# Kernel optimization log

Hardware: AMD Instinct MI355X
Metric: run time of the kernel (lower is better)

The kernel has to match this reference:

```python
import jax, jax.numpy as jnp
import numpy as np


def _conv1x1(x, w, b):
    # x: [B, Cin, H, W]; w: [Cout, Cin, 1, 1]; b: [Cout]
    y = jnp.einsum('bchw,oc->bohw', x, w[:, :, 0, 0])
    return y + b[None, :, None, None]


def setup_inputs() -> dict:
    key = jax.random.key(0)
    ks = jax.random.split(key, 9)
    B, C, H, W = 8, 256, 64, 64
    Cq = C // 4
    sc = 0.05
    return {
        'x': jax.random.normal(ks[0], (B, C, H, W), jnp.float32),
        'query_weight': jax.random.normal(ks[1], (Cq, C, 1, 1), jnp.float32) * sc,
        'query_bias': jax.random.normal(ks[2], (Cq,), jnp.float32) * sc,
        'key_weight': jax.random.normal(ks[3], (Cq, C, 1, 1), jnp.float32) * sc,
        'key_bias': jax.random.normal(ks[4], (Cq,), jnp.float32) * sc,
        'value_weight': jax.random.normal(ks[5], (C, C, 1, 1), jnp.float32) * sc,
        'value_bias': jax.random.normal(ks[6], (C,), jnp.float32) * sc,
        'gamma_weight': jax.random.normal(ks[7], (C, C, 1, 1), jnp.float32) * sc,
        'gamma_bias': jax.random.normal(ks[8], (C,), jnp.float32) * sc,
    }


def reference(x, query_weight, query_bias, key_weight, key_bias,
              value_weight, value_bias, gamma_weight, gamma_bias):
    B, C, H, W = x.shape
    N = H * W
    q = _conv1x1(x, query_weight, query_bias).reshape(B, -1, N)   # [B, Cq, N]
    k = _conv1x1(x, key_weight, key_bias).reshape(B, -1, N)       # [B, Cq, N]
    v = _conv1x1(x, value_weight, value_bias).reshape(B, C, N)    # [B, C, N]
    # energy[b, i, j] = sum_c q[b, c, i] * k[b, c, j]
    energy = jnp.einsum('bci,bcj->bij', q, k)                     # [B, N, N]
    energy = jax.nn.elu(energy) / N
    out = jnp.einsum('bcn,bnm->bcm', v, energy).reshape(B, C, H, W)
    return _conv1x1(out, gamma_weight, gamma_bias)
```

## Files before the change

kernel.cpp:

```cpp
#include <hip/hip_runtime.h>
#include <cmath>

#define BB 8
#define CC 256
#define CQ 64
#define NN 4096
#define VROW 4224
constexpr float INV_N = 1.0f / 4096.0f;

typedef __attribute__((ext_vector_type(8))) short short8;
typedef __attribute__((ext_vector_type(4))) short short4v;
typedef __attribute__((ext_vector_type(4))) float float4v;

__device__ __forceinline__ short f2bf(float f) {
  union { float f; unsigned u; } x; x.f = f;
  unsigned r = x.u + 0x7fffu + ((x.u >> 16) & 1u);
  return (short)(r >> 16);
}

__device__ __forceinline__ void lds_barrier() {
  asm volatile("s_waitcnt lgkmcnt(0)" ::: "memory");
  __builtin_amdgcn_s_barrier();
  __builtin_amdgcn_sched_barrier(0);
}

__global__ void wconv_kernel(const float* __restrict__ wq,
                             const float* __restrict__ wk,
                             short* __restrict__ wqb, short* __restrict__ wkb) {
  const int t = blockIdx.x * 256 + threadIdx.x;
  const float* src; short* dst; int idx;
  if (t < 4096) { src = wq; dst = wqb; idx = t; }
  else          { src = wk; dst = wkb; idx = t - 4096; }
  const float4 v = *reinterpret_cast<const float4*>(&src[(size_t)idx * 4]);
  short4v o;
  o[0] = f2bf(v.x); o[1] = f2bf(v.y); o[2] = f2bf(v.z); o[3] = f2bf(v.w);
  *reinterpret_cast<short4v*>(&dst[(size_t)idx * 4]) = o;
}

__global__ void wprep_kernel(const float* __restrict__ wg,
                             const float* __restrict__ wv,
                             const float* __restrict__ bv,
                             short* __restrict__ wvpb, float* __restrict__ bvp) {
  const int o = blockIdx.x, t = threadIdx.x;
  float s = 0.f;
  for (int c = 0; c < 256; ++c)
    s += wg[(size_t)o * 256 + c] * wv[(size_t)c * 256 + t];
  wvpb[(size_t)o * 256 + t] = f2bf(s);

  __shared__ float red[256];
  red[t] = wg[(size_t)o * 256 + t] * bv[t];
  __syncthreads();
  for (int off = 128; off; off >>= 1) {
    if (t < off) red[t] += red[t + off];
    __syncthreads();
  }
  if (t == 0) bvp[o] = red[0];
}

__global__ __launch_bounds__(256, 2) void qkv_kernel(
    const float* __restrict__ X,
    const short* __restrict__ wqb, const float* __restrict__ bq,
    const short* __restrict__ wkb, const float* __restrict__ bk,
    const short* __restrict__ wvpb, const float* __restrict__ bvp,
    short* __restrict__ qt, short* __restrict__ kt, short* __restrict__ vbf) {
  __shared__ short xt[64 * 264];
  const int tid = threadIdx.x;
  const int wid = tid >> 6;
  const int lane = tid & 63, quad = lane >> 4, l16 = lane & 15;
  const int b = blockIdx.x, n0 = blockIdx.y * 64;

  float4 xb[16];
#pragma unroll
  for (int p = 0; p < 16; ++p) {
    const int idx = p * 256 + tid;
    const int c = idx >> 4;
    const int n4 = (idx & 15) * 4;
    xb[p] = *reinterpret_cast<const float4*>(
        &X[((size_t)b * CC + c) * NN + n0 + n4]);
  }
#pragma unroll
  for (int p = 0; p < 16; ++p) {
    const int idx = p * 256 + tid;
    const int c = idx >> 4;
    const int n4 = (idx & 15) * 4;
    xt[(n4 + 0) * 264 + c] = f2bf(xb[p].x);
    xt[(n4 + 1) * 264 + c] = f2bf(xb[p].y);
    xt[(n4 + 2) * 264 + c] = f2bf(xb[p].z);
    xt[(n4 + 3) * 264 + c] = f2bf(xb[p].w);
  }
  __syncthreads();

  short8 bfr[8][4];
#pragma unroll
  for (int kk = 0; kk < 8; ++kk)
#pragma unroll
    for (int tm = 0; tm < 4; ++tm)
      bfr[kk][tm] = *reinterpret_cast<const short8*>(
          &xt[(tm * 16 + l16) * 264 + kk * 32 + quad * 8]);
  __syncthreads();

  short* Os0 = xt;
  short* Os1 = xt + 4608;

  for (int ch = 0; ch < 6; ++ch) {
    const short* W; const float* bias; int obase;
    if (ch == 0)      { W = wqb; bias = bq; obase = 0; }
    else if (ch == 1) { W = wkb; bias = bk; obase = 0; }
    else { W = wvpb + (size_t)(ch - 2) * 64 * CC; bias = bvp + (ch - 2) * 64; obase = (ch - 2) * 64; }

    const short* wrow = &W[(size_t)(wid * 16 + l16) * CC + quad * 8];
    short8 wf[8];
#pragma unroll
    for (int kk = 0; kk < 8; ++kk)
      wf[kk] = *reinterpret_cast<const short8*>(wrow + kk * 32);

    float4v acc[4];
#pragma unroll
    for (int tm = 0; tm < 4; ++tm) acc[tm] = float4v{0.f, 0.f, 0.f, 0.f};
#pragma unroll
    for (int kk = 0; kk < 8; ++kk)
#pragma unroll
      for (int tm = 0; tm < 4; ++tm)
        acc[tm] = __builtin_amdgcn_mfma_f32_16x16x32_bf16(wf[kk], bfr[kk][tm], acc[tm], 0, 0, 0);

    if (ch < 2) {
      short* dst = (ch == 0) ? qt : kt;
#pragma unroll
      for (int tm = 0; tm < 4; ++tm) {
        short4v pk;
#pragma unroll
        for (int r = 0; r < 4; ++r)
          pk[r] = f2bf(acc[tm][r] + bias[wid * 16 + quad * 4 + r]);
        *reinterpret_cast<short4v*>(
            &dst[((size_t)b * NN + n0 + tm * 16 + l16) * 64 + wid * 16 + quad * 4]) = pk;
      }
    } else {
      short* Os = (ch & 1) ? Os1 : Os0;
#pragma unroll
      for (int tm = 0; tm < 4; ++tm)
#pragma unroll
        for (int r = 0; r < 4; ++r)
          Os[(wid * 16 + quad * 4 + r) * 72 + tm * 16 + l16] =
              f2bf(acc[tm][r] + bias[wid * 16 + quad * 4 + r]);
      __syncthreads();
      const int o = tid >> 2, ng = (tid & 3) * 16;
      const int orow = obase + o;
      const short8 s0 = *reinterpret_cast<const short8*>(&Os[o * 72 + ng]);
      const short8 s1 = *reinterpret_cast<const short8*>(&Os[o * 72 + ng + 8]);
      short* vp = &vbf[((size_t)b * CC + orow) * VROW + n0 + ng];
      *reinterpret_cast<short8*>(vp) = s0;
      *reinterpret_cast<short8*>(vp + 8) = s1;
    }
  }
}

__global__ __launch_bounds__(256, 2) void attn_kernel(
    const short* __restrict__ qt, const short* __restrict__ kt,
    const short* __restrict__ vbf, const float* __restrict__ bg,
    float* __restrict__ out) {
  __shared__ short smem[9216];
  short* Es0 = smem;
  short* Es1 = smem + 4608;

  const int tid = threadIdx.x;
  const int wid = tid >> 6;
  const int lane = tid & 63, quad = lane >> 4, l16 = lane & 15;
  const int b = blockIdx.x, m0 = blockIdx.y * 64;

  short8 bkf[4][2];
#pragma unroll
  for (int tm = 0; tm < 4; ++tm)
#pragma unroll
    for (int kk = 0; kk < 2; ++kk)
      bkf[tm][kk] = *reinterpret_cast<const short8*>(
          &kt[((size_t)b * NN + m0 + tm * 16 + l16) * 64 + kk * 32 + quad * 8]);

  const short* qp = &qt[((size_t)b * NN + wid * 16 + l16) * 64 + quad * 8];
  const short* vrow[4];
#pragma unroll
  for (int tc = 0; tc < 4; ++tc) {
    const int crow = wid * 64 + tc * 16 + l16;
    vrow[tc] = &vbf[((size_t)b * CC + crow) * VROW + quad * 8];
  }

  float4v acc[4][4];
#pragma unroll
  for (int i = 0; i < 4; ++i)
#pragma unroll
    for (int j = 0; j < 4; ++j) acc[i][j] = float4v{0.f, 0.f, 0.f, 0.f};

  short8 avA[4][2], avB[4][2];
#pragma unroll
  for (int tc = 0; tc < 4; ++tc) {
    avA[tc][0] = *reinterpret_cast<const short8*>(vrow[tc]);
    avA[tc][1] = *reinterpret_cast<const short8*>(vrow[tc] + 32);
  }
  short8 aqA0 = *reinterpret_cast<const short8*>(qp + (size_t)1 * 4096);
  short8 aqA1 = *reinterpret_cast<const short8*>(qp + (size_t)1 * 4096 + 32);
  short8 aqB0, aqB1;
  {
    const short8 aq0 = *reinterpret_cast<const short8*>(qp);
    const short8 aq1 = *reinterpret_cast<const short8*>(qp + 32);
#pragma unroll
    for (int tm = 0; tm < 4; ++tm) {
      float4v t = {0.f, 0.f, 0.f, 0.f};
      t = __builtin_amdgcn_mfma_f32_16x16x32_bf16(aq0, bkf[tm][0], t, 0, 0, 0);
      t = __builtin_amdgcn_mfma_f32_16x16x32_bf16(aq1, bkf[tm][1], t, 0, 0, 0);
      short4v pk;
#pragma unroll
      for (int r = 0; r < 4; ++r) {
        float sv = t[r];
        sv = (sv > 0.f) ? sv : (__expf(sv) - 1.f);
        pk[r] = f2bf(sv);
      }
      *reinterpret_cast<short4v*>(
          &Es0[(tm * 16 + l16) * 72 + wid * 16 + quad * 4]) = pk;
    }
  }
  lds_barrier();

  auto seg = [&](int it, short8 (&avc)[4][2], short8 (&avn)[4][2],
                 short8& aqc0, short8& aqc1, short8& aqn0, short8& aqn1) {
    const int nb1 = (it + 1) * 64;
#pragma unroll
    for (int tc = 0; tc < 4; ++tc) {
      avn[tc][0] = *reinterpret_cast<const short8*>(vrow[tc] + nb1);
      avn[tc][1] = *reinterpret_cast<const short8*>(vrow[tc] + nb1 + 32);
    }
    aqn0 = *reinterpret_cast<const short8*>(qp + (size_t)(it + 2) * 4096);
    aqn1 = *reinterpret_cast<const short8*>(qp + (size_t)(it + 2) * 4096 + 32);

    short* Esr = (it & 1) ? Es1 : Es0;
    short* Esw = (it & 1) ? Es0 : Es1;

    float4v s[4];
    if (it < 63) {
#pragma unroll
      for (int tm = 0; tm < 4; ++tm) {
        float4v t = {0.f, 0.f, 0.f, 0.f};
        t = __builtin_amdgcn_mfma_f32_16x16x32_bf16(aqc0, bkf[tm][0], t, 0, 0, 0);
        t = __builtin_amdgcn_mfma_f32_16x16x32_bf16(aqc1, bkf[tm][1], t, 0, 0, 0);
        s[tm] = t;
      }
    }

#pragma unroll
    for (int tm = 0; tm < 4; ++tm) {
      const short8 be0 = *reinterpret_cast<const short8*>(
          &Esr[(tm * 16 + l16) * 72 + quad * 8]);
      const short8 be1 = *reinterpret_cast<const short8*>(
          &Esr[(tm * 16 + l16) * 72 + 32 + quad * 8]);
#pragma unroll
      for (int tc = 0; tc < 4; ++tc) {
        acc[tc][tm] = __builtin_amdgcn_mfma_f32_16x16x32_bf16(avc[tc][0], be0, acc[tc][tm], 0, 0, 0);
        acc[tc][tm] = __builtin_amdgcn_mfma_f32_16x16x32_bf16(avc[tc][1], be1, acc[tc][tm], 0, 0, 0);
      }
    }

    if (it < 63) {
#pragma unroll
      for (int tm = 0; tm < 4; ++tm) {
        short4v pk;
#pragma unroll
        for (int r = 0; r < 4; ++r) {
          float sv = s[tm][r];
          sv = (sv > 0.f) ? sv : (__expf(sv) - 1.f);
          pk[r] = f2bf(sv);
        }
        *reinterpret_cast<short4v*>(
            &Esw[(tm * 16 + l16) * 72 + wid * 16 + quad * 4]) = pk;
      }
    }
    lds_barrier();
  };

  for (int it = 0; it < 64; it += 2) {
    seg(it,     avA, avB, aqA0, aqA1, aqB0, aqB1);
    seg(it + 1, avB, avA, aqB0, aqB1, aqA0, aqA1);
  }

#pragma unroll
  for (int tc = 0; tc < 4; ++tc) {
#pragma unroll
    for (int r = 0; r < 4; ++r) {
      const int o = wid * 64 + tc * 16 + quad * 4 + r;
      const float bgv = bg[o];
#pragma unroll
      for (int tm = 0; tm < 4; ++tm) {
        out[((size_t)b * CC + o) * NN + m0 + tm * 16 + l16] =
            acc[tc][tm][r] * INV_N + bgv;
      }
    }
  }
}

extern "C" void kernel_launch(void* const* d_in, const int* in_sizes, int n_in,
                              void* d_out, int out_size, void* d_ws,
                              size_t ws_size, hipStream_t stream) {
  const float* x  = (const float*)d_in[0];
  const float* wq = (const float*)d_in[1];
  const float* bq = (const float*)d_in[2];
  const float* wk = (const float*)d_in[3];
  const float* bk = (const float*)d_in[4];
  const float* wv = (const float*)d_in[5];
  const float* bv = (const float*)d_in[6];
  const float* wg = (const float*)d_in[7];
  const float* bg = (const float*)d_in[8];
  float* out = (float*)d_out;

  short* qt   = (short*)d_ws;
  short* kt   = qt + (size_t)BB * NN * CQ;
  short* vbf  = kt + (size_t)BB * NN * CQ;
  short* wqb  = vbf + (size_t)BB * CC * VROW;
  short* wkb  = wqb + (size_t)CQ * CC;
  short* wvpb = wkb + (size_t)CQ * CC;
  float* bvp  = (float*)(wvpb + (size_t)CC * CC);

  wconv_kernel<<<dim3(32), 256, 0, stream>>>(wq, wk, wqb, wkb);
  wprep_kernel<<<dim3(256), 256, 0, stream>>>(wg, wv, bv, wvpb, bvp);
  qkv_kernel<<<dim3(BB, NN / 64), 256, 0, stream>>>(x, wqb, bq, wkb, bk,
                                                    wvpb, bvp, qt, kt, vbf);
  attn_kernel<<<dim3(BB, NN / 64), 256, 0, stream>>>(qt, kt, vbf, bg, out);
}
```

Before: 274.7 us.

## Keep energy tiles in registers and drop LDS staging and barriers

The attention kernel no longer has its four waves cooperatively compute the energy tile, write it to double-buffered LDS and synchronise with barriers. Each wave now recomputes the whole 64x64 energy tile itself, loading Q rows in a permuted order so the MFMA output layout lines up with the B-operand layout of the next MFMA. This removes LDS traffic and block-wide barriers. In exchange each wave does four times the QK MFMA and exp work, and the software prefetch of V and Q into registers is gone.

After: 355.4 us. +29.4%, slower.

```diff
diff --git a/kernel.cpp b/kernel.cpp
--- a/kernel.cpp
+++ b/kernel.cpp
@@ -16,12 +16,6 @@
   union { float f; unsigned u; } x; x.f = f;
   unsigned r = x.u + 0x7fffu + ((x.u >> 16) & 1u);
   return (short)(r >> 16);
-}
-
-__device__ __forceinline__ void lds_barrier() {
-  asm volatile("s_waitcnt lgkmcnt(0)" ::: "memory");
-  __builtin_amdgcn_s_barrier();
-  __builtin_amdgcn_sched_barrier(0);
 }
 
 __global__ void wconv_kernel(const float* __restrict__ wq,
@@ -158,10 +152,6 @@
     const short* __restrict__ qt, const short* __restrict__ kt,
     const short* __restrict__ vbf, const float* __restrict__ bg,
     float* __restrict__ out) {
-  __shared__ short smem[9216];
-  short* Es0 = smem;
-  short* Es1 = smem + 4608;
-
   const int tid = threadIdx.x;
   const int wid = tid >> 6;
   const int lane = tid & 63, quad = lane >> 4, l16 = lane & 15;
@@ -171,17 +161,20 @@
 #pragma unroll
   for (int tm = 0; tm < 4; ++tm)
 #pragma unroll
-    for (int kk = 0; kk < 2; ++kk)
-      bkf[tm][kk] = *reinterpret_cast<const short8*>(
-          &kt[((size_t)b * NN + m0 + tm * 16 + l16) * 64 + kk * 32 + quad * 8]);
-
-  const short* qp = &qt[((size_t)b * NN + wid * 16 + l16) * 64 + quad * 8];
+    for (int ch = 0; ch < 2; ++ch)
+      bkf[tm][ch] = *reinterpret_cast<const short8*>(
+          &kt[((size_t)b * NN + m0 + tm * 16 + l16) * 64 + ch * 32 + quad * 8]);
+
+  int nperm[4];
+#pragma unroll
+  for (int ng = 0; ng < 4; ++ng)
+    nperm[ng] = (ng & 2) * 16 + (l16 >> 2) * 8 + (ng & 1) * 4 + (l16 & 3);
+  const short* qbase = &qt[(size_t)b * NN * 64 + quad * 8];
+
   const short* vrow[4];
 #pragma unroll
-  for (int tc = 0; tc < 4; ++tc) {
-    const int crow = wid * 64 + tc * 16 + l16;
-    vrow[tc] = &vbf[((size_t)b * CC + crow) * VROW + quad * 8];
-  }
+  for (int tc = 0; tc < 4; ++tc)
+    vrow[tc] = &vbf[((size_t)b * CC + wid * 64 + tc * 16 + l16) * VROW + quad * 8];
 
   float4v acc[4][4];
 #pragma unroll
@@ -189,94 +182,55 @@
 #pragma unroll
     for (int j = 0; j < 4; ++j) acc[i][j] = float4v{0.f, 0.f, 0.f, 0.f};
 
-  short8 avA[4][2], avB[4][2];
-#pragma unroll
-  for (int tc = 0; tc < 4; ++tc) {
-    avA[tc][0] = *reinterpret_cast<const short8*>(vrow[tc]);
-    avA[tc][1] = *reinterpret_cast<const short8*>(vrow[tc] + 32);
-  }
-  short8 aqA0 = *reinterpret_cast<const short8*>(qp + (size_t)1 * 4096);
-  short8 aqA1 = *reinterpret_cast<const short8*>(qp + (size_t)1 * 4096 + 32);
-  short8 aqB0, aqB1;
-  {
-    const short8 aq0 = *reinterpret_cast<const short8*>(qp);
-    const short8 aq1 = *reinterpret_cast<const short8*>(qp + 32);
+  for (int it = 0; it < 64; ++it) {
+    const int nb = it * 64;
+
+    short8 aq[4][2];
+#pragma unroll
+    for (int ng = 0; ng < 4; ++ng) {
+      const short* qp = qbase + (size_t)(nb + nperm[ng]) * 64;
+      aq[ng][0] = *reinterpret_cast<const short8*>(qp);
+      aq[ng][1] = *reinterpret_cast<const short8*>(qp + 32);
+    }
+    short8 av[4][2];
+#pragma unroll
+    for (int tc = 0; tc < 4; ++tc) {
+      av[tc][0] = *reinterpret_cast<const short8*>(vrow[tc] + nb);
+      av[tc][1] = *reinterpret_cast<const short8*>(vrow[tc] + nb + 32);
+    }
+
 #pragma unroll
     for (int tm = 0; tm < 4; ++tm) {
-      float4v t = {0.f, 0.f, 0.f, 0.f};
-      t = __builtin_amdgcn_mfma_f32_16x16x32_bf16(aq0, bkf[tm][0], t, 0, 0, 0);
-      t = __builtin_amdgcn_mfma_f32_16x16x32_bf16(aq1, bkf[tm][1], t, 0, 0, 0);
-      short4v pk;
+      float4v s[4];
+#pragma unroll
+      for (int ng = 0; ng < 4; ++ng) {
+        float4v t = {0.f, 0.f, 0.f, 0.f};
+        t = __builtin_amdgcn_mfma_f32_16x16x32_bf16(aq[ng][0], bkf[tm][0], t, 0, 0, 0);
+        t = __builtin_amdgcn_mfma_f32_16x16x32_bf16(aq[ng][1], bkf[tm][1], t, 0, 0, 0);
+        s[ng] = t;
+      }
+      short8 e0, e1;
 #pragma unroll
       for (int r = 0; r < 4; ++r) {
-        float sv = t[r];
-        sv = (sv > 0.f) ? sv : (__expf(sv) - 1.f);
-        pk[r] = f2bf(sv);
-      }
-      *reinterpret_cast<short4v*>(
-          &Es0[(tm * 16 + l16) * 72 + wid * 16 + quad * 4]) = pk;
-    }
-  }
-  lds_barrier();
-
-  auto seg = [&](int it, short8 (&avc)[4][2], short8 (&avn)[4][2],
-                 short8& aqc0, short8& aqc1, short8& aqn0, short8& aqn1) {
-    const int nb1 = (it + 1) * 64;
-#pragma unroll
-    for (int tc = 0; tc < 4; ++tc) {
-      avn[tc][0] = *reinterpret_cast<const short8*>(vrow[tc] + nb1);
-      avn[tc][1] = *reinterpret_cast<const short8*>(vrow[tc] + nb1 + 32);
-    }
-    aqn0 = *reinterpret_cast<const short8*>(qp + (size_t)(it + 2) * 4096);
-    aqn1 = *reinterpret_cast<const short8*>(qp + (size_t)(it + 2) * 4096 + 32);
-
-    short* Esr = (it & 1) ? Es1 : Es0;
-    short* Esw = (it & 1) ? Es0 : Es1;
-
-    float4v s[4];
-    if (it < 63) {
-#pragma unroll
-      for (int tm = 0; tm < 4; ++tm) {
-        float4v t = {0.f, 0.f, 0.f, 0.f};
-        t = __builtin_amdgcn_mfma_f32_16x16x32_bf16(aqc0, bkf[tm][0], t, 0, 0, 0);
-        t = __builtin_amdgcn_mfma_f32_16x16x32_bf16(aqc1, bkf[tm][1], t, 0, 0, 0);
-        s[tm] = t;
-      }
-    }
-
-#pragma unroll
-    for (int tm = 0; tm < 4; ++tm) {
-      const short8 be0 = *reinterpret_cast<const short8*>(
-          &Esr[(tm * 16 + l16) * 72 + quad * 8]);
-      const short8 be1 = *reinterpret_cast<const short8*>(
-          &Esr[(tm * 16 + l16) * 72 + 32 + quad * 8]);
+        float v0 = s[0][r];
+        v0 = (v0 > 0.f) ? v0 : (__expf(v0) - 1.f);
+        e0[r] = f2bf(v0);
+        float v1 = s[1][r];
+        v1 = (v1 > 0.f) ? v1 : (__expf(v1) - 1.f);
+        e0[4 + r] = f2bf(v1);
+        float v2 = s[2][r];
+        v2 = (v2 > 0.f) ? v2 : (__expf(v2) - 1.f);
+        e1[r] = f2bf(v2);
+        float v3 = s[3][r];
+        v3 = (v3 > 0.f) ? v3 : (__expf(v3) - 1.f);
+        e1[4 + r] = f2bf(v3);
+      }
 #pragma unroll
       for (int tc = 0; tc < 4; ++tc) {
-        acc[tc][tm] = __builtin_amdgcn_mfma_f32_16x16x32_bf16(avc[tc][0], be0, acc[tc][tm], 0, 0, 0);
-        acc[tc][tm] = __builtin_amdgcn_mfma_f32_16x16x32_bf16(avc[tc][1], be1, acc[tc][tm], 0, 0, 0);
-      }
-    }
-
-    if (it < 63) {
-#pragma unroll
-      for (int tm = 0; tm < 4; ++tm) {
-        short4v pk;
-#pragma unroll
-        for (int r = 0; r < 4; ++r) {
-          float sv = s[tm][r];
-          sv = (sv > 0.f) ? sv : (__expf(sv) - 1.f);
-          pk[r] = f2bf(sv);
-        }
-        *reinterpret_cast<short4v*>(
-            &Esw[(tm * 16 + l16) * 72 + wid * 16 + quad * 4]) = pk;
-      }
-    }
-    lds_barrier();
-  };
-
-  for (int it = 0; it < 64; it += 2) {
-    seg(it,     avA, avB, aqA0, aqA1, aqB0, aqB1);
-    seg(it + 1, avB, avA, aqB0, aqB1, aqA0, aqA1);
+        acc[tc][tm] = __builtin_amdgcn_mfma_f32_16x16x32_bf16(av[tc][0], e0, acc[tc][tm], 0, 0, 0);
+        acc[tc][tm] = __builtin_amdgcn_mfma_f32_16x16x32_bf16(av[tc][1], e1, acc[tc][tm], 0, 0, 0);
+      }
+    }
   }
 
 #pragma unroll
```

## Warp-specialize attention kernel into energy producer and value consumer waves

Applied to the files above, without the earlier changes.

The attention kernel now launches 512 threads per block. Four waves compute QK^T energy with ELU and write it to double-buffered LDS, while four other waves read that energy and run the V·E MFMA accumulation. Consumer waves raise their priority with s_setprio during the MFMA phase. The aim is to overlap the energy computation and its exp with the main matmul instead of serializing them within each wave. In exchange it doubles the threads per block and changes launch bounds, which may limit occupancy, and the two roles stay coupled by a block barrier every iteration.

Result: slower. 404.3 us (+47.2%).

```diff
diff --git a/kernel.cpp b/kernel.cpp
--- a/kernel.cpp
+++ b/kernel.cpp
@@ -154,7 +154,7 @@
   }
 }
 
-__global__ __launch_bounds__(256, 2) void attn_kernel(
+__global__ __launch_bounds__(512, 4) void attn_kernel(
     const short* __restrict__ qt, const short* __restrict__ kt,
     const short* __restrict__ vbf, const float* __restrict__ bg,
     float* __restrict__ out) {
@@ -167,128 +167,130 @@
   const int lane = tid & 63, quad = lane >> 4, l16 = lane & 15;
   const int b = blockIdx.x, m0 = blockIdx.y * 64;
 
-  short8 bkf[4][2];
-#pragma unroll
-  for (int tm = 0; tm < 4; ++tm)
-#pragma unroll
-    for (int kk = 0; kk < 2; ++kk)
-      bkf[tm][kk] = *reinterpret_cast<const short8*>(
-          &kt[((size_t)b * NN + m0 + tm * 16 + l16) * 64 + kk * 32 + quad * 8]);
-
-  const short* qp = &qt[((size_t)b * NN + wid * 16 + l16) * 64 + quad * 8];
-  const short* vrow[4];
-#pragma unroll
-  for (int tc = 0; tc < 4; ++tc) {
-    const int crow = wid * 64 + tc * 16 + l16;
-    vrow[tc] = &vbf[((size_t)b * CC + crow) * VROW + quad * 8];
-  }
-
-  float4v acc[4][4];
-#pragma unroll
-  for (int i = 0; i < 4; ++i)
-#pragma unroll
-    for (int j = 0; j < 4; ++j) acc[i][j] = float4v{0.f, 0.f, 0.f, 0.f};
-
-  short8 avA[4][2], avB[4][2];
-#pragma unroll
-  for (int tc = 0; tc < 4; ++tc) {
-    avA[tc][0] = *reinterpret_cast<const short8*>(vrow[tc]);
-    avA[tc][1] = *reinterpret_cast<const short8*>(vrow[tc] + 32);
-  }
-  short8 aqA0 = *reinterpret_cast<const short8*>(qp + (size_t)1 * 4096);
-  short8 aqA1 = *reinterpret_cast<const short8*>(qp + (size_t)1 * 4096 + 32);
-  short8 aqB0, aqB1;
-  {
-    const short8 aq0 = *reinterpret_cast<const short8*>(qp);
-    const short8 aq1 = *reinterpret_cast<const short8*>(qp + 32);
-#pragma unroll
-    for (int tm = 0; tm < 4; ++tm) {
-      float4v t = {0.f, 0.f, 0.f, 0.f};
-      t = __builtin_amdgcn_mfma_f32_16x16x32_bf16(aq0, bkf[tm][0], t, 0, 0, 0);
-      t = __builtin_amdgcn_mfma_f32_16x16x32_bf16(aq1, bkf[tm][1], t, 0, 0, 0);
-      short4v pk;
-#pragma unroll
-      for (int r = 0; r < 4; ++r) {
-        float sv = t[r];
-        sv = (sv > 0.f) ? sv : (__expf(sv) - 1.f);
-        pk[r] = f2bf(sv);
-      }
-      *reinterpret_cast<short4v*>(
-          &Es0[(tm * 16 + l16) * 72 + wid * 16 + quad * 4]) = pk;
-    }
-  }
-  lds_barrier();
-
-  auto seg = [&](int it, short8 (&avc)[4][2], short8 (&avn)[4][2],
-                 short8& aqc0, short8& aqc1, short8& aqn0, short8& aqn1) {
-    const int nb1 = (it + 1) * 64;
-#pragma unroll
-    for (int tc = 0; tc < 4; ++tc) {
-      avn[tc][0] = *reinterpret_cast<const short8*>(vrow[tc] + nb1);
-      avn[tc][1] = *reinterpret_cast<const short8*>(vrow[tc] + nb1 + 32);
-    }
-    aqn0 = *reinterpret_cast<const short8*>(qp + (size_t)(it + 2) * 4096);
-    aqn1 = *reinterpret_cast<const short8*>(qp + (size_t)(it + 2) * 4096 + 32);
-
-    short* Esr = (it & 1) ? Es1 : Es0;
-    short* Esw = (it & 1) ? Es0 : Es1;
-
-    float4v s[4];
-    if (it < 63) {
+  if (wid < 4) {
+    const int ns = wid;
+    short8 bkf[4][2];
+#pragma unroll
+    for (int tm = 0; tm < 4; ++tm)
+#pragma unroll
+      for (int ch = 0; ch < 2; ++ch)
+        bkf[tm][ch] = *reinterpret_cast<const short8*>(
+            &kt[((size_t)b * NN + m0 + tm * 16 + l16) * 64 + ch * 32 + quad * 8]);
+
+    const short* qp = &qt[((size_t)b * NN + ns * 16 + l16) * 64 + quad * 8];
+
+    {
+      const short8 a0 = *reinterpret_cast<const short8*>(qp);
+      const short8 a1 = *reinterpret_cast<const short8*>(qp + 32);
 #pragma unroll
       for (int tm = 0; tm < 4; ++tm) {
         float4v t = {0.f, 0.f, 0.f, 0.f};
-        t = __builtin_amdgcn_mfma_f32_16x16x32_bf16(aqc0, bkf[tm][0], t, 0, 0, 0);
-        t = __builtin_amdgcn_mfma_f32_16x16x32_bf16(aqc1, bkf[tm][1], t, 0, 0, 0);
-        s[tm] = t;
-      }
-    }
-
-#pragma unroll
-    for (int tm = 0; tm < 4; ++tm) {
-      const short8 be0 = *reinterpret_cast<const short8*>(
-          &Esr[(tm * 16 + l16) * 72 + quad * 8]);
-      const short8 be1 = *reinterpret_cast<const short8*>(
-          &Esr[(tm * 16 + l16) * 72 + 32 + quad * 8]);
-#pragma unroll
-      for (int tc = 0; tc < 4; ++tc) {
-        acc[tc][tm] = __builtin_amdgcn_mfma_f32_16x16x32_bf16(avc[tc][0], be0, acc[tc][tm], 0, 0, 0);
-        acc[tc][tm] = __builtin_amdgcn_mfma_f32_16x16x32_bf16(avc[tc][1], be1, acc[tc][tm], 0, 0, 0);
-      }
-    }
-
-    if (it < 63) {
-#pragma unroll
-      for (int tm = 0; tm < 4; ++tm) {
+        t = __builtin_amdgcn_mfma_f32_16x16x32_bf16(a0, bkf[tm][0], t, 0, 0, 0);
+        t = __builtin_amdgcn_mfma_f32_16x16x32_bf16(a1, bkf[tm][1], t, 0, 0, 0);
         short4v pk;
 #pragma unroll
         for (int r = 0; r < 4; ++r) {
-          float sv = s[tm][r];
+          float sv = t[r];
           sv = (sv > 0.f) ? sv : (__expf(sv) - 1.f);
           pk[r] = f2bf(sv);
         }
         *reinterpret_cast<short4v*>(
-            &Esw[(tm * 16 + l16) * 72 + wid * 16 + quad * 4]) = pk;
-      }
-    }
+            &Es0[(tm * 16 + l16) * 72 + ns * 16 + quad * 4]) = pk;
+      }
+    }
+    short8 aqA0 = *reinterpret_cast<const short8*>(qp + (size_t)4096);
+    short8 aqA1 = *reinterpret_cast<const short8*>(qp + (size_t)4096 + 32);
+    short8 aqB0, aqB1;
     lds_barrier();
-  };
-
-  for (int it = 0; it < 64; it += 2) {
-    seg(it,     avA, avB, aqA0, aqA1, aqB0, aqB1);
-    seg(it + 1, avB, avA, aqB0, aqB1, aqA0, aqA1);
-  }
-
-#pragma unroll
-  for (int tc = 0; tc < 4; ++tc) {
-#pragma unroll
-    for (int r = 0; r < 4; ++r) {
-      const int o = wid * 64 + tc * 16 + quad * 4 + r;
-      const float bgv = bg[o];
+
+    auto pseg = [&](int it, short8& c0, short8& c1, short8& n0_, short8& n1_) {
+      n0_ = *reinterpret_cast<const short8*>(qp + (size_t)(it + 2) * 4096);
+      n1_ = *reinterpret_cast<const short8*>(qp + (size_t)(it + 2) * 4096 + 32);
+      if (it < 63) {
+        short* Esw = ((it + 1) & 1) ? Es1 : Es0;
+#pragma unroll
+        for (int tm = 0; tm < 4; ++tm) {
+          float4v t = {0.f, 0.f, 0.f, 0.f};
+          t = __builtin_amdgcn_mfma_f32_16x16x32_bf16(c0, bkf[tm][0], t, 0, 0, 0);
+          t = __builtin_amdgcn_mfma_f32_16x16x32_bf16(c1, bkf[tm][1], t, 0, 0, 0);
+          short4v pk;
+#pragma unroll
+          for (int r = 0; r < 4; ++r) {
+            float sv = t[r];
+            sv = (sv > 0.f) ? sv : (__expf(sv) - 1.f);
+            pk[r] = f2bf(sv);
+          }
+          *reinterpret_cast<short4v*>(
+              &Esw[(tm * 16 + l16) * 72 + ns * 16 + quad * 4]) = pk;
+        }
+      }
+      lds_barrier();
+    };
+    for (int it = 0; it < 64; it += 2) {
+      pseg(it,     aqA0, aqA1, aqB0, aqB1);
+      pseg(it + 1, aqB0, aqB1, aqA0, aqA1);
+    }
+  } else {
+    const int cw = wid - 4;
+    const short* vrow[4];
+#pragma unroll
+    for (int tc = 0; tc < 4; ++tc)
+      vrow[tc] = &vbf[((size_t)b * CC + cw * 64 + tc * 16 + l16) * VROW + quad * 8];
+
+    float4v acc[4][4];
+#pragma unroll
+    for (int i = 0; i < 4; ++i)
+#pragma unroll
+      for (int j = 0; j < 4; ++j) acc[i][j] = float4v{0.f, 0.f, 0.f, 0.f};
+
+    short8 avA[4][2], avB[4][2];
+#pragma unroll
+    for (int tc = 0; tc < 4; ++tc) {
+      avA[tc][0] = *reinterpret_cast<const short8*>(vrow[tc]);
+      avA[tc][1] = *reinterpret_cast<const short8*>(vrow[tc] + 32);
+    }
+    lds_barrier();
+
+    auto cseg = [&](int it, short8 (&avc)[4][2], short8 (&avn)[4][2]) {
+      const int nb1 = (it + 1) * 64;
+#pragma unroll
+      for (int tc = 0; tc < 4; ++tc) {
+        avn[tc][0] = *reinterpret_cast<const short8*>(vrow[tc] + nb1);
+        avn[tc][1] = *reinterpret_cast<const short8*>(vrow[tc] + nb1 + 32);
+      }
+      short* Esr = (it & 1) ? Es1 : Es0;
+      __builtin_amdgcn_s_setprio(1);
 #pragma unroll
       for (int tm = 0; tm < 4; ++tm) {
-        out[((size_t)b * CC + o) * NN + m0 + tm * 16 + l16] =
-            acc[tc][tm][r] * INV_N + bgv;
+        const short8 be0 = *reinterpret_cast<const short8*>(
+            &Esr[(tm * 16 + l16) * 72 + quad * 8]);
+        const short8 be1 = *reinterpret_cast<const short8*>(
+            &Esr[(tm * 16 + l16) * 72 + 32 + quad * 8]);
+#pragma unroll
+        for (int tc = 0; tc < 4; ++tc) {
+          acc[tc][tm] = __builtin_amdgcn_mfma_f32_16x16x32_bf16(avc[tc][0], be0, acc[tc][tm], 0, 0, 0);
+          acc[tc][tm] = __builtin_amdgcn_mfma_f32_16x16x32_bf16(avc[tc][1], be1, acc[tc][tm], 0, 0, 0);
+        }
+      }
+      __builtin_amdgcn_s_setprio(0);
+      lds_barrier();
+    };
+    for (int it = 0; it < 64; it += 2) {
+      cseg(it,     avA, avB);
+      cseg(it + 1, avB, avA);
+    }
+
+#pragma unroll
+    for (int tc = 0; tc < 4; ++tc) {
+#pragma unroll
+      for (int r = 0; r < 4; ++r) {
+        const int o = cw * 64 + tc * 16 + quad * 4 + r;
+        const float bgv = bg[o];
+#pragma unroll
+        for (int tm = 0; tm < 4; ++tm) {
+          out[((size_t)b * CC + o) * NN + m0 + tm * 16 + l16] =
+              acc[tc][tm][r] * INV_N + bgv;
+        }
       }
     }
   }
@@ -320,5 +322,5 @@
   wprep_kernel<<<dim3(256), 256, 0, stream>>>(wg, wv, bv, wvpb, bvp);
   qkv_kernel<<<dim3(BB, NN / 64), 256, 0, stream>>>(x, wqb, bq, wkb, bk,
                                                     wvpb, bvp, qt, kt, vbf);
-  attn_kernel<<<dim3(BB, NN / 64), 256, 0, stream>>>(qt, kt, vbf, bg, out);
-}
+  attn_kernel<<<dim3(BB, NN / 64), 512, 0, stream>>>(qt, kt, vbf, bg, out);
+}
```

## Stage V tiles through padded shared memory with cooperative coalesced loads

Applied to the files above, without the earlier changes.

The attention kernel no longer has each wave load its V operand fragments straight from global memory into registers. All 256 threads now cooperatively load a 256x64 V tile with row-contiguous accesses into a padded shared buffer, and the MFMA loop reads its A fragments from there. The aim is better global coalescing and fewer registers held for double-buffered V fragments. The cost is extra shared-memory traffic, a second barrier per iteration, much larger shared usage, and 66-element row padding that leaves 16-byte vector accesses only 4-byte aligned.

Result: slower. 394.2 us (+43.5%).

```diff
diff --git a/kernel.cpp b/kernel.cpp
--- a/kernel.cpp
+++ b/kernel.cpp
@@ -6,6 +6,7 @@
 #define CQ 64
 #define NN 4096
 #define VROW 4224
+#define VSP 66
 constexpr float INV_N = 1.0f / 4096.0f;
 
 typedef __attribute__((ext_vector_type(8))) short short8;
@@ -158,30 +159,28 @@
     const short* __restrict__ qt, const short* __restrict__ kt,
     const short* __restrict__ vbf, const float* __restrict__ bg,
     float* __restrict__ out) {
-  __shared__ short smem[9216];
-  short* Es0 = smem;
-  short* Es1 = smem + 4608;
+  __shared__ short smem[26112];
+  short* Vs  = smem;
+  short* Es0 = smem + 16896;
+  short* Es1 = smem + 21504;
 
   const int tid = threadIdx.x;
   const int wid = tid >> 6;
   const int lane = tid & 63, quad = lane >> 4, l16 = lane & 15;
   const int b = blockIdx.x, m0 = blockIdx.y * 64;
 
+  const int srow = tid >> 3, scol = (tid & 7) * 8;
+  const short* vsrc = &vbf[((size_t)b * CC + srow) * VROW + scol];
+
   short8 bkf[4][2];
 #pragma unroll
   for (int tm = 0; tm < 4; ++tm)
 #pragma unroll
-    for (int kk = 0; kk < 2; ++kk)
-      bkf[tm][kk] = *reinterpret_cast<const short8*>(
-          &kt[((size_t)b * NN + m0 + tm * 16 + l16) * 64 + kk * 32 + quad * 8]);
+    for (int ch = 0; ch < 2; ++ch)
+      bkf[tm][ch] = *reinterpret_cast<const short8*>(
+          &kt[((size_t)b * NN + m0 + tm * 16 + l16) * 64 + ch * 32 + quad * 8]);
 
   const short* qp = &qt[((size_t)b * NN + wid * 16 + l16) * 64 + quad * 8];
-  const short* vrow[4];
-#pragma unroll
-  for (int tc = 0; tc < 4; ++tc) {
-    const int crow = wid * 64 + tc * 16 + l16;
-    vrow[tc] = &vbf[((size_t)b * CC + crow) * VROW + quad * 8];
-  }
 
   float4v acc[4][4];
 #pragma unroll
@@ -189,23 +188,21 @@
 #pragma unroll
     for (int j = 0; j < 4; ++j) acc[i][j] = float4v{0.f, 0.f, 0.f, 0.f};
 
-  short8 avA[4][2], avB[4][2];
-#pragma unroll
-  for (int tc = 0; tc < 4; ++tc) {
-    avA[tc][0] = *reinterpret_cast<const short8*>(vrow[tc]);
-    avA[tc][1] = *reinterpret_cast<const short8*>(vrow[tc] + 32);
-  }
-  short8 aqA0 = *reinterpret_cast<const short8*>(qp + (size_t)1 * 4096);
-  short8 aqA1 = *reinterpret_cast<const short8*>(qp + (size_t)1 * 4096 + 32);
+  short8 vst[8];
+#pragma unroll
+  for (int p = 0; p < 8; ++p)
+    vst[p] = *reinterpret_cast<const short8*>(vsrc + (size_t)(32 * p) * VROW);
+  short8 aqA0 = *reinterpret_cast<const short8*>(qp + (size_t)4096);
+  short8 aqA1 = *reinterpret_cast<const short8*>(qp + (size_t)4096 + 32);
   short8 aqB0, aqB1;
   {
-    const short8 aq0 = *reinterpret_cast<const short8*>(qp);
-    const short8 aq1 = *reinterpret_cast<const short8*>(qp + 32);
+    const short8 a0 = *reinterpret_cast<const short8*>(qp);
+    const short8 a1 = *reinterpret_cast<const short8*>(qp + 32);
 #pragma unroll
     for (int tm = 0; tm < 4; ++tm) {
       float4v t = {0.f, 0.f, 0.f, 0.f};
-      t = __builtin_amdgcn_mfma_f32_16x16x32_bf16(aq0, bkf[tm][0], t, 0, 0, 0);
-      t = __builtin_amdgcn_mfma_f32_16x16x32_bf16(aq1, bkf[tm][1], t, 0, 0, 0);
+      t = __builtin_amdgcn_mfma_f32_16x16x32_bf16(a0, bkf[tm][0], t, 0, 0, 0);
+      t = __builtin_amdgcn_mfma_f32_16x16x32_bf16(a1, bkf[tm][1], t, 0, 0, 0);
       short4v pk;
 #pragma unroll
       for (int r = 0; r < 4; ++r) {
@@ -217,24 +214,25 @@
           &Es0[(tm * 16 + l16) * 72 + wid * 16 + quad * 4]) = pk;
     }
   }
+#pragma unroll
+  for (int p = 0; p < 8; ++p)
+    *reinterpret_cast<short8*>(&Vs[(srow + 32 * p) * VSP + scol]) = vst[p];
   lds_barrier();
 
-  auto seg = [&](int it, short8 (&avc)[4][2], short8 (&avn)[4][2],
-                 short8& aqc0, short8& aqc1, short8& aqn0, short8& aqn1) {
+  auto seg = [&](int it, short8& aqc0, short8& aqc1, short8& aqn0, short8& aqn1) {
     const int nb1 = (it + 1) * 64;
 #pragma unroll
-    for (int tc = 0; tc < 4; ++tc) {
-      avn[tc][0] = *reinterpret_cast<const short8*>(vrow[tc] + nb1);
-      avn[tc][1] = *reinterpret_cast<const short8*>(vrow[tc] + nb1 + 32);
-    }
+    for (int p = 0; p < 8; ++p)
+      vst[p] = *reinterpret_cast<const short8*>(
+          vsrc + (size_t)(32 * p) * VROW + nb1);
     aqn0 = *reinterpret_cast<const short8*>(qp + (size_t)(it + 2) * 4096);
     aqn1 = *reinterpret_cast<const short8*>(qp + (size_t)(it + 2) * 4096 + 32);
 
     short* Esr = (it & 1) ? Es1 : Es0;
     short* Esw = (it & 1) ? Es0 : Es1;
 
-    float4v s[4];
     if (it < 63) {
+      float4v s[4];
 #pragma unroll
       for (int tm = 0; tm < 4; ++tm) {
         float4v t = {0.f, 0.f, 0.f, 0.f};
@@ -242,22 +240,6 @@
         t = __builtin_amdgcn_mfma_f32_16x16x32_bf16(aqc1, bkf[tm][1], t, 0, 0, 0);
         s[tm] = t;
       }
-    }
-
-#pragma unroll
-    for (int tm = 0; tm < 4; ++tm) {
-      const short8 be0 = *reinterpret_cast<const short8*>(
-          &Esr[(tm * 16 + l16) * 72 + quad * 8]);
-      const short8 be1 = *reinterpret_cast<const short8*>(
-          &Esr[(tm * 16 + l16) * 72 + 32 + quad * 8]);
-#pragma unroll
-      for (int tc = 0; tc < 4; ++tc) {
-        acc[tc][tm] = __builtin_amdgcn_mfma_f32_16x16x32_bf16(avc[tc][0], be0, acc[tc][tm], 0, 0, 0);
-        acc[tc][tm] = __builtin_amdgcn_mfma_f32_16x16x32_bf16(avc[tc][1], be1, acc[tc][tm], 0, 0, 0);
-      }
-    }
-
-    if (it < 63) {
 #pragma unroll
       for (int tm = 0; tm < 4; ++tm) {
         short4v pk;
@@ -272,11 +254,34 @@
       }
     }
     lds_barrier();
+
+#pragma unroll
+    for (int tm = 0; tm < 4; ++tm) {
+      const short8 be0 = *reinterpret_cast<const short8*>(
+          &Esr[(tm * 16 + l16) * 72 + quad * 8]);
+      const short8 be1 = *reinterpret_cast<const short8*>(
+          &Esr[(tm * 16 + l16) * 72 + 32 + quad * 8]);
+#pragma unroll
+      for (int tc = 0; tc < 4; ++tc) {
+        const int cr = wid * 64 + tc * 16 + l16;
+        const short8 a0 = *reinterpret_cast<const short8*>(
+            &Vs[cr * VSP + quad * 8]);
+        const short8 a1 = *reinterpret_cast<const short8*>(
+            &Vs[cr * VSP + 32 + quad * 8]);
+        acc[tc][tm] = __builtin_amdgcn_mfma_f32_16x16x32_bf16(a0, be0, acc[tc][tm], 0, 0, 0);
+        acc[tc][tm] = __builtin_amdgcn_mfma_f32_16x16x32_bf16(a1, be1, acc[tc][tm], 0, 0, 0);
+      }
+    }
+    lds_barrier();
+
+#pragma unroll
+    for (int p = 0; p < 8; ++p)
+      *reinterpret_cast<short8*>(&Vs[(srow + 32 * p) * VSP + scol]) = vst[p];
   };
 
   for (int it = 0; it < 64; it += 2) {
-    seg(it,     avA, avB, aqA0, aqA1, aqB0, aqB1);
-    seg(it + 1, avB, avA, aqB0, aqB1, aqA0, aqA1);
+    seg(it,     aqA0, aqA1, aqB0, aqB1);
+    seg(it + 1, aqB0, aqB1, aqA0, aqA1);
   }
 
 #pragma unroll
```
